# Optimization experiments

Hardware: AMD Instinct MI355X
Metric: run time of the kernel (lower is better)

The kernel has to match this reference:

```python
import jax, jax.numpy as jnp
import numpy as np

EPS = 1e-7  # keras.backend.epsilon()


def setup_inputs() -> dict:
    key = jax.random.key(0)
    kx, kw, ku = jax.random.split(key, 3)
    B, S, F = 16, 4096, 512
    x = jax.random.normal(kx, (B, S, F), dtype=jnp.float32)
    # glorot-uniform-scaled weights
    limW = np.sqrt(6.0 / (F + F)).astype(np.float32)
    W = jax.random.uniform(kw, (F, F), dtype=jnp.float32, minval=-limW, maxval=limW)
    b = jnp.zeros((F,), dtype=jnp.float32)
    limu = np.sqrt(6.0 / (F + 1)).astype(np.float32)
    u = jax.random.uniform(ku, (F,), dtype=jnp.float32, minval=-limu, maxval=limu)
    return {"x": x, "W": W, "b": b, "u": u}


def reference(x, W, b, u):
    # x: [B,S,F]  W: [F,F]  b: [F]  u: [F]
    h = jnp.tanh(jnp.einsum('bsf,fg->bsg', x, W) + b)   # [B,S,F]
    scores = jnp.einsum('bsf,f->bs', h, u)              # [B,S]
    e = jnp.exp(scores)
    # NOTE: faithful to the source, normalization is GLOBAL over all B*S scores
    a = e / (jnp.sum(e) + EPS)                          # [B,S]
    out = jnp.einsum('bsf,bs->bf', x, a)                # [B,F] weighted-sum pool over steps
    return out
```

## Files before the change

kernel.cpp:

```cpp
#include <hip/hip_runtime.h>
#include <stdint.h>

#define EPSV 1e-7f
#define FDIM 512
#define ROWS 128
#define BK 64
#define NROWS 65536

typedef __bf16 bf16_t;
typedef bf16_t bf16x8 __attribute__((ext_vector_type(8)));
typedef unsigned short ushort8 __attribute__((ext_vector_type(8)));
typedef float f32x4 __attribute__((ext_vector_type(4)));

#define AS1 __attribute__((address_space(1)))
#define AS3 __attribute__((address_space(3)))

__device__ __forceinline__ unsigned short f2bf(float f) {
  union { float f; unsigned int u; } c; c.f = f;
  unsigned int u = c.u;
  unsigned int r = u + 0x7fffu + ((u >> 16) & 1u);
  return (unsigned short)(r >> 16);
}
__device__ __forceinline__ float bf2f(unsigned short s) {
  union { unsigned int u; float f; } c; c.u = ((unsigned int)s) << 16;
  return c.f;
}

__device__ __forceinline__ float fast_tanh(float x) {
  x = fminf(15.0f, fmaxf(-15.0f, x));
  float t = __expf(2.0f * x);
  return 1.0f - 2.0f * __builtin_amdgcn_rcpf(t + 1.0f);
}

__global__ void convert_W(const float* __restrict__ W, unsigned short* __restrict__ Wt) {
  __shared__ unsigned short tile[32][34];
  const int t = threadIdx.x;
  const int tx = t & 31, ty = t >> 5;
  const int bn = blockIdx.x & 15, bk = blockIdx.x >> 4;
  const int k0 = bk * 32, n0 = bn * 32;
#pragma unroll
  for (int i = 0; i < 4; ++i) {
    int r = ty + i * 8;
    tile[r][tx] = f2bf(W[(size_t)(k0 + r) * FDIM + n0 + tx]);
  }
  __syncthreads();
#pragma unroll
  for (int i = 0; i < 4; ++i) {
    int r = ty + i * 8;
    Wt[(size_t)(n0 + r) * FDIM + k0 + tx] = tile[tx][r];
  }
}

#define ISSUE_B(col0_, kb_)                                                    \
  do {                                                                         \
    _Pragma("unroll") for (int i_ = 0; i_ < 2; ++i_) {                         \
      const int rb_ = w * 16 + i_ * 8;                                         \
      const int rl_ = rb_ + (lane >> 3);                                       \
      const int j_ = (lane & 7) ^ (rl_ & 7);                                   \
      const unsigned short* g_ =                                               \
          Wt + (size_t)((col0_) + rl_) * FDIM + (kb_) + j_ * 8;                \
      unsigned short* l_ = (unsigned short*)(sB + rb_ * BK);                   \
      __builtin_amdgcn_global_load_lds((AS1 void*)(g_), (AS3 void*)(l_), 16,   \
                                       0, 0);                                  \
    }                                                                          \
  } while (0)

__global__ __launch_bounds__(512, 2) void fused_score_pool(
    const float* __restrict__ x, const unsigned short* __restrict__ Wt,
    const float* __restrict__ bvec, const float* __restrict__ uvec,
    float* __restrict__ ppool, float* __restrict__ sumE) {
  __shared__ alignas(16) unsigned short sA[ROWS * FDIM];
  __shared__ alignas(16) unsigned short sB[128 * BK];
  __shared__ float score_s[ROWS];
  __shared__ float e_s[ROWS];

  const int t = threadIdx.x;
  const int lane = t & 63;
  const int w = t >> 6;
  const int wm = w & 1;
  const int wn = w >> 1;
  const int quad = lane >> 4;
  const int l15 = lane & 15;
  const int m0 = blockIdx.x * ROWS;

  if (t < ROWS) score_s[t] = 0.0f;

  ISSUE_B(0, 0);

#pragma unroll
  for (int p = 0; p < 16; ++p) {
    const int row = p * 8 + w;
    const float* g = x + (size_t)(m0 + row) * FDIM + lane * 8;
    float4 lo = *(const float4*)g;
    float4 hi = *(const float4*)(g + 4);
    ushort8 v;
    v[0] = f2bf(lo.x); v[1] = f2bf(lo.y); v[2] = f2bf(lo.z); v[3] = f2bf(lo.w);
    v[4] = f2bf(hi.x); v[5] = f2bf(hi.y); v[6] = f2bf(hi.z); v[7] = f2bf(hi.w);
    const int jp = lane ^ (row & 7);
    *(ushort8*)(void*)(sA + row * FDIM + jp * 8) = v;
  }
  __syncthreads();

  float sc[4][4];
#pragma unroll
  for (int mi = 0; mi < 4; ++mi)
#pragma unroll
    for (int r = 0; r < 4; ++r) sc[mi][r] = 0.0f;

  for (int nc = 0; nc < 4; ++nc) {
    const int col0 = nc * 128;
    f32x4 acc[4][2];
#pragma unroll
    for (int mi = 0; mi < 4; ++mi)
#pragma unroll
      for (int ni = 0; ni < 2; ++ni) acc[mi][ni] = (f32x4){0.f, 0.f, 0.f, 0.f};

    for (int kc = 0; kc < 8; ++kc) {
      bf16x8 bfr[2][2];
#pragma unroll
      for (int ni = 0; ni < 2; ++ni)
#pragma unroll
        for (int ks = 0; ks < 2; ++ks) {
          const int nrow = wn * 32 + ni * 16 + l15;
          const int phys = (ks * 4 + quad) ^ (nrow & 7);
          bfr[ni][ks] = *(const bf16x8*)(const void*)(sB + nrow * BK + phys * 8);
        }
      __syncthreads();

      const int s = nc * 8 + kc + 1;
      if (s < 32) ISSUE_B((s >> 3) * 128, (s & 7) * BK);

#pragma unroll
      for (int ks = 0; ks < 2; ++ks) {
        bf16x8 af[4];
#pragma unroll
        for (int mi = 0; mi < 4; ++mi) {
          const int row = wm * 64 + mi * 16 + l15;
          const int phys = kc * 8 + ((ks * 4 + quad) ^ (row & 7));
          af[mi] = *(const bf16x8*)(const void*)(sA + row * FDIM + phys * 8);
        }
#pragma unroll
        for (int mi = 0; mi < 4; ++mi)
#pragma unroll
          for (int ni = 0; ni < 2; ++ni)
            acc[mi][ni] = __builtin_amdgcn_mfma_f32_16x16x32_bf16(
                af[mi], bfr[ni][ks], acc[mi][ni], 0, 0, 0);
      }
      __syncthreads();
    }

#pragma unroll
    for (int ni = 0; ni < 2; ++ni) {
      const int cl = col0 + wn * 32 + ni * 16 + l15;
      const float uu = uvec[cl], bb = bvec[cl];
#pragma unroll
      for (int mi = 0; mi < 4; ++mi)
#pragma unroll
        for (int r = 0; r < 4; ++r)
          sc[mi][r] += uu * fast_tanh(acc[mi][ni][r] + bb);
    }
  }

#pragma unroll
  for (int mi = 0; mi < 4; ++mi)
#pragma unroll
    for (int r = 0; r < 4; ++r) {
      float v = sc[mi][r];
      v += __shfl_xor(v, 1); v += __shfl_xor(v, 2);
      v += __shfl_xor(v, 4); v += __shfl_xor(v, 8);
      if (l15 == 0)
        atomicAdd(&score_s[wm * 64 + mi * 16 + quad * 4 + r], v);
    }
  __syncthreads();

  if (t < ROWS) {
    const float e = __expf(score_s[t]);
    e_s[t] = e;
    float v = e;
    v += __shfl_xor(v, 1);  v += __shfl_xor(v, 2);  v += __shfl_xor(v, 4);
    v += __shfl_xor(v, 8);  v += __shfl_xor(v, 16); v += __shfl_xor(v, 32);
    if (lane == 0) atomicAdd(sumE, v);
  }
  __syncthreads();

  float a[8];
#pragma unroll
  for (int jj = 0; jj < 8; ++jj) a[jj] = 0.0f;
#pragma unroll
  for (int rr = 0; rr < 16; ++rr) {
    const int row = w * 16 + rr;
    const int jp = lane ^ (row & 7);
    const ushort8 v = *(const ushort8*)(const void*)(sA + row * FDIM + jp * 8);
    const float wg = e_s[row];
#pragma unroll
    for (int jj = 0; jj < 8; ++jj) a[jj] += bf2f(v[jj]) * wg;
  }
  float* red = (float*)sB;
  *(float4*)&red[w * FDIM + lane * 8]     = (float4){a[0], a[1], a[2], a[3]};
  *(float4*)&red[w * FDIM + lane * 8 + 4] = (float4){a[4], a[5], a[6], a[7]};
  __syncthreads();
  {
    float sv = 0.0f;
#pragma unroll
    for (int g = 0; g < 8; ++g) sv += red[g * FDIM + t];
    ppool[(size_t)blockIdx.x * FDIM + t] = sv;
  }
}

__global__ __launch_bounds__(256) void finalize(
    const float* __restrict__ ppool, const float* __restrict__ sumE,
    float* __restrict__ out) {
  const int i = blockIdx.x * 256 + threadIdx.x;
  const int b = i >> 9, f = i & 511;
  const float* p = ppool + (size_t)b * 32 * FDIM + f;
  float s = 0.0f;
#pragma unroll
  for (int c = 0; c < 32; ++c) s += p[(size_t)c * FDIM];
  out[i] = s / (*sumE + EPSV);
}

extern "C" void kernel_launch(void* const* d_in, const int* in_sizes, int n_in,
                              void* d_out, int out_size, void* d_ws, size_t ws_size,
                              hipStream_t stream) {
  (void)in_sizes; (void)n_in; (void)out_size; (void)ws_size;
  const float* x = (const float*)d_in[0];
  const float* W = (const float*)d_in[1];
  const float* b = (const float*)d_in[2];
  const float* u = (const float*)d_in[3];
  float* out = (float*)d_out;

  char* p = (char*)d_ws;
  unsigned short* Wt = (unsigned short*)p;  p += (size_t)FDIM * FDIM * 2;
  float* sumE = (float*)p;                  p += 256;
  float* ppool = (float*)p;                 p += (size_t)(NROWS / ROWS) * FDIM * 4;

  hipMemsetAsync(sumE, 0, sizeof(float), stream);
  convert_W<<<dim3(256), dim3(256), 0, stream>>>(W, Wt);
  fused_score_pool<<<dim3(NROWS / ROWS), dim3(512), 0, stream>>>(
      x, Wt, b, u, ppool, sumE);
  finalize<<<dim3(32), dim3(256), 0, stream>>>(ppool, sumE, out);
}
```

Measured before the change: 258.2 us.

## Double-buffer W tiles with wider column passes and fold memset into convert kernel

Restructures the GEMM loop to process 256 output columns per pass with a 32-wide K step and a double-buffered B tile in LDS, issuing the next tile's async load before computing the current one. This halves the barriers per step and doubles the MFMA work per A-fragment load. Score scratch arrays are aliased onto the B buffer to keep LDS within budget, and the sumE zeroing moves from a memset into convert_W to drop a launch. Costs are more accumulator registers and LDS usage right at the limit.

```diff
diff --git a/kernel.cpp b/kernel.cpp
--- a/kernel.cpp
+++ b/kernel.cpp
@@ -4,7 +4,8 @@
 #define EPSV 1e-7f
 #define FDIM 512
 #define ROWS 128
-#define BK 64
+#define BK 32
+#define PCOLS 256
 #define NROWS 65536
 
 typedef __bf16 bf16_t;
@@ -32,7 +33,9 @@
   return 1.0f - 2.0f * __builtin_amdgcn_rcpf(t + 1.0f);
 }
 
-__global__ void convert_W(const float* __restrict__ W, unsigned short* __restrict__ Wt) {
+__global__ void convert_W(const float* __restrict__ W, unsigned short* __restrict__ Wt,
+                          float* __restrict__ sumE) {
+  if (blockIdx.x == 0 && threadIdx.x == 0) *sumE = 0.0f;
   __shared__ unsigned short tile[32][34];
   const int t = threadIdx.x;
   const int tx = t & 31, ty = t >> 5;
@@ -51,15 +54,15 @@
   }
 }
 
-#define ISSUE_B(col0_, kb_)                                                    \
+#define ISSUE_B(buf_, pass_, kc_)                                              \
   do {                                                                         \
     _Pragma("unroll") for (int i_ = 0; i_ < 2; ++i_) {                         \
-      const int rb_ = w * 16 + i_ * 8;                                         \
-      const int rl_ = rb_ + (lane >> 3);                                       \
-      const int j_ = (lane & 7) ^ (rl_ & 7);                                   \
+      const int rb_ = (w * 2 + i_) * 16;                                       \
+      const int rl_ = rb_ + (lane >> 2);                                       \
+      const int j_ = (lane & 3) ^ ((rl_ >> 2) & 3);                            \
       const unsigned short* g_ =                                               \
-          Wt + (size_t)((col0_) + rl_) * FDIM + (kb_) + j_ * 8;                \
-      unsigned short* l_ = (unsigned short*)(sB + rb_ * BK);                   \
+          Wt + (size_t)((pass_) * PCOLS + rl_) * FDIM + (kc_) * BK + j_ * 8;   \
+      unsigned short* l_ = (unsigned short*)(&sB[buf_][0] + rb_ * BK);         \
       __builtin_amdgcn_global_load_lds((AS1 void*)(g_), (AS3 void*)(l_), 16,   \
                                        0, 0);                                  \
     }                                                                          \
@@ -70,9 +73,7 @@
     const float* __restrict__ bvec, const float* __restrict__ uvec,
     float* __restrict__ ppool, float* __restrict__ sumE) {
   __shared__ alignas(16) unsigned short sA[ROWS * FDIM];
-  __shared__ alignas(16) unsigned short sB[128 * BK];
-  __shared__ float score_s[ROWS];
-  __shared__ float e_s[ROWS];
+  __shared__ alignas(16) unsigned short sB[2][PCOLS * BK];
 
   const int t = threadIdx.x;
   const int lane = t & 63;
@@ -83,9 +84,7 @@
   const int l15 = lane & 15;
   const int m0 = blockIdx.x * ROWS;
 
-  if (t < ROWS) score_s[t] = 0.0f;
-
-  ISSUE_B(0, 0);
+  ISSUE_B(0, 0, 0);
 
 #pragma unroll
   for (int p = 0; p < 16; ++p) {
@@ -107,51 +106,48 @@
 #pragma unroll
     for (int r = 0; r < 4; ++r) sc[mi][r] = 0.0f;
 
-  for (int nc = 0; nc < 4; ++nc) {
-    const int col0 = nc * 128;
-    f32x4 acc[4][2];
+  int cur = 0;
+  for (int pass = 0; pass < 2; ++pass) {
+    f32x4 acc[4][4];
 #pragma unroll
     for (int mi = 0; mi < 4; ++mi)
 #pragma unroll
-      for (int ni = 0; ni < 2; ++ni) acc[mi][ni] = (f32x4){0.f, 0.f, 0.f, 0.f};
-
-    for (int kc = 0; kc < 8; ++kc) {
-      bf16x8 bfr[2][2];
-#pragma unroll
-      for (int ni = 0; ni < 2; ++ni)
-#pragma unroll
-        for (int ks = 0; ks < 2; ++ks) {
-          const int nrow = wn * 32 + ni * 16 + l15;
-          const int phys = (ks * 4 + quad) ^ (nrow & 7);
-          bfr[ni][ks] = *(const bf16x8*)(const void*)(sB + nrow * BK + phys * 8);
-        }
+      for (int ni = 0; ni < 4; ++ni) acc[mi][ni] = (f32x4){0.f, 0.f, 0.f, 0.f};
+
+#pragma unroll 2
+    for (int kc = 0; kc < 16; ++kc) {
+      const int s = pass * 16 + kc + 1;
+      if (s < 32) ISSUE_B(cur ^ 1, (s >> 4), (s & 15));
+
+      bf16x8 bfr[4], af[4];
+#pragma unroll
+      for (int ni = 0; ni < 4; ++ni) {
+        const int r = wn * 64 + ni * 16 + l15;
+        const int phys = quad ^ ((r >> 2) & 3);
+        bfr[ni] = *(const bf16x8*)(const void*)(&sB[cur][0] + r * BK + phys * 8);
+      }
+#pragma unroll
+      for (int mi = 0; mi < 4; ++mi) {
+        const int row = wm * 64 + mi * 16 + l15;
+        const int g = kc * 4 + quad;
+        const int phys = g ^ (row & 7);
+        af[mi] = *(const bf16x8*)(const void*)(sA + row * FDIM + phys * 8);
+      }
+
+#pragma unroll
+      for (int mi = 0; mi < 4; ++mi)
+#pragma unroll
+        for (int ni = 0; ni < 4; ++ni)
+          acc[mi][ni] = __builtin_amdgcn_mfma_f32_16x16x32_bf16(
+              af[mi], bfr[ni], acc[mi][ni], 0, 0, 0);
+
       __syncthreads();
-
-      const int s = nc * 8 + kc + 1;
-      if (s < 32) ISSUE_B((s >> 3) * 128, (s & 7) * BK);
-
-#pragma unroll
-      for (int ks = 0; ks < 2; ++ks) {
-        bf16x8 af[4];
-#pragma unroll
-        for (int mi = 0; mi < 4; ++mi) {
-          const int row = wm * 64 + mi * 16 + l15;
-          const int phys = kc * 8 + ((ks * 4 + quad) ^ (row & 7));
-          af[mi] = *(const bf16x8*)(const void*)(sA + row * FDIM + phys * 8);
-        }
-#pragma unroll
-        for (int mi = 0; mi < 4; ++mi)
-#pragma unroll
-          for (int ni = 0; ni < 2; ++ni)
-            acc[mi][ni] = __builtin_amdgcn_mfma_f32_16x16x32_bf16(
-                af[mi], bfr[ni][ks], acc[mi][ni], 0, 0, 0);
-      }
-      __syncthreads();
+      cur ^= 1;
     }
 
 #pragma unroll
-    for (int ni = 0; ni < 2; ++ni) {
-      const int cl = col0 + wn * 32 + ni * 16 + l15;
+    for (int ni = 0; ni < 4; ++ni) {
+      const int cl = pass * PCOLS + wn * 64 + ni * 16 + l15;
       const float uu = uvec[cl], bb = bvec[cl];
 #pragma unroll
       for (int mi = 0; mi < 4; ++mi)
@@ -160,6 +156,14 @@
           sc[mi][r] += uu * fast_tanh(acc[mi][ni][r] + bb);
     }
   }
+
+  float* sBf = (float*)&sB[0][0];
+  float* red = sBf;
+  float* score_s = sBf + 4096;
+  float* e_s = sBf + 4096 + 128;
+
+  if (t < ROWS) score_s[t] = 0.0f;
+  __syncthreads();
 
 #pragma unroll
   for (int mi = 0; mi < 4; ++mi)
@@ -195,7 +199,6 @@
 #pragma unroll
     for (int jj = 0; jj < 8; ++jj) a[jj] += bf2f(v[jj]) * wg;
   }
-  float* red = (float*)sB;
   *(float4*)&red[w * FDIM + lane * 8]     = (float4){a[0], a[1], a[2], a[3]};
   *(float4*)&red[w * FDIM + lane * 8 + 4] = (float4){a[4], a[5], a[6], a[7]};
   __syncthreads();
@@ -234,8 +237,7 @@
   float* sumE = (float*)p;                  p += 256;
   float* ppool = (float*)p;                 p += (size_t)(NROWS / ROWS) * FDIM * 4;
 
-  hipMemsetAsync(sumE, 0, sizeof(float), stream);
-  convert_W<<<dim3(256), dim3(256), 0, stream>>>(W, Wt);
+  convert_W<<<dim3(256), dim3(256), 0, stream>>>(W, Wt, sumE);
   fused_score_pool<<<dim3(NROWS / ROWS), dim3(512), 0, stream>>>(
       x, Wt, b, u, ppool, sumE);
   finalize<<<dim3(32), dim3(256), 0, stream>>>(ppool, sumE, out);
```

Result: faster. 248.8 us (-3.6%).
